# Optimization experiments

Measured on AMD Instinct MI355X. Metric: run time of the kernel, lower is better.

Reference implementation:

```python
import jax, jax.numpy as jnp
import numpy as np

B, N, ND, H = 8, 1024, 64, 128
NUM_OPS, NUM_PARAMS, SKETCH = 64, 256, 128


def setup_inputs() -> dict:
    key = jax.random.key(0)
    ks = iter(jax.random.split(key, 64))

    def rn(shape, s=0.05):
        return jax.random.normal(next(ks), shape, dtype=jnp.float32) * s

    inp = {
        'node_features': jax.random.normal(next(ks), (B, N, ND), dtype=jnp.float32),
        'adjacency': (jax.random.uniform(next(ks), (B, N, N)) < 0.05).astype(jnp.float32),
        'mask': jnp.ones((B, N), jnp.float32),
    }
    for name, din in (('g1', ND), ('g2', H), ('g3', H)):
        inp[name + '_W'] = rn((din, H))
        inp[name + '_b'] = jnp.zeros((H,), jnp.float32)
        inp[name + '_aW'] = rn((2 * H,))
        inp[name + '_ab'] = jnp.zeros((), jnp.float32)
    for l in (0, 1):
        inp[f'l{l}_Wih'] = rn((4 * H, H))
        inp[f'l{l}_Whh'] = rn((4 * H, H))
        inp[f'l{l}_bih'] = jnp.zeros((4 * H,), jnp.float32)
        inp[f'l{l}_bhh'] = jnp.zeros((4 * H,), jnp.float32)
    for name, dout in (('op', NUM_OPS), ('pa', NUM_PARAMS), ('sk', SKETCH), ('no', ND)):
        inp[name + '_W1'] = rn((H, H))
        inp[name + '_b1'] = jnp.zeros((H,), jnp.float32)
        inp[name + '_W2'] = rn((H, dout))
        inp[name + '_b2'] = jnp.zeros((dout,), jnp.float32)
    return inp


def _gnn(x, adj, W, b, aW, ab):
    # h = Linear(x); att[b,i,j] = sigmoid(aW . [h_j ; h_i] + ab)  (cat order from the torch code)
    h = x @ W + b                      # [B,N,H]
    D = W.shape[1]
    sj = h @ aW[:D]                    # contribution of the dim-1-expanded term (h_j)
    si = h @ aW[D:]                    # contribution of the dim-2-expanded term (h_i)
    att = jax.nn.sigmoid(si[:, :, None] + sj[:, None, :] + ab) * adj  # [B,N,N]
    return jnp.einsum('bij,bjd->bid', att, h)


def _lstm(x, Wih, Whh, bih, bhh):
    # single torch-style LSTM layer, gate order i,f,g,o; zero initial state
    Bx, Hh = x.shape[0], Whh.shape[1]

    def step(carry, xt):
        h, c = carry
        g = xt @ Wih.T + h @ Whh.T + (bih + bhh)       # [B,4H]
        i, f, gg, o = jnp.split(g, 4, axis=-1)
        c = jax.nn.sigmoid(f) * c + jax.nn.sigmoid(i) * jnp.tanh(gg)
        h = jax.nn.sigmoid(o) * jnp.tanh(c)
        return (h, c), h

    z = jnp.zeros((Bx, Hh), x.dtype)
    _, ys = jax.lax.scan(step, (z, z), jnp.swapaxes(x, 0, 1))
    return jnp.swapaxes(ys, 0, 1)


def _mlp(x, W1, b1, W2, b2):
    return jax.nn.relu(x @ W1 + b1) @ W2 + b2


def reference(node_features, adjacency, mask,
              g1_W, g1_b, g1_aW, g1_ab,
              g2_W, g2_b, g2_aW, g2_ab,
              g3_W, g3_b, g3_aW, g3_ab,
              l0_Wih, l0_Whh, l0_bih, l0_bhh,
              l1_Wih, l1_Whh, l1_bih, l1_bhh,
              op_W1, op_b1, op_W2, op_b2,
              pa_W1, pa_b1, pa_W2, pa_b2,
              sk_W1, sk_b1, sk_W2, sk_b2,
              no_W1, no_b1, no_W2, no_b2):
    h = jax.nn.relu(_gnn(node_features, adjacency, g1_W, g1_b, g1_aW, g1_ab))
    h = jax.nn.relu(_gnn(h, adjacency, g2_W, g2_b, g2_aW, g2_ab))
    h = _gnn(h, adjacency, g3_W, g3_b, g3_aW, g3_ab)
    lo = _lstm(h, l0_Wih, l0_Whh, l0_bih, l0_bhh)
    lo = _lstm(lo, l1_Wih, l1_Whh, l1_bih, l1_bhh)
    op_pred = _mlp(lo, op_W1, op_b1, op_W2, op_b2)
    param_pred = _mlp(lo, pa_W1, pa_b1, pa_W2, pa_b2)
    sketch_pred = _mlp(lo, sk_W1, sk_b1, sk_W2, sk_b2)
    node_pred = _mlp(h, no_W1, no_b1, no_W2, no_b2)
    return (op_pred, param_pred, sketch_pred, node_pred)
```

## Files before the change

### kernel.cpp

```cpp
#include <hip/hip_runtime.h>
#include <hip/hip_fp16.h>

typedef __attribute__((ext_vector_type(8))) short short8;
typedef __attribute__((ext_vector_type(4))) float f32x4;
typedef __attribute__((ext_vector_type(2))) unsigned int u32x2;

__device__ __forceinline__ unsigned short bf16_of(float f) {
    unsigned u = __builtin_bit_cast(unsigned, f);
    u += 0x7fffu + ((u >> 16) & 1u);
    return (unsigned short)(u >> 16);
}
__device__ __forceinline__ unsigned bf16pk(float a, float b) {
    return (unsigned)bf16_of(a) | ((unsigned)bf16_of(b) << 16);
}
__device__ __forceinline__ unsigned fp16pk(float a, float b) {
    return __builtin_bit_cast(unsigned, __builtin_amdgcn_cvt_pkrtz(a, b));
}
__device__ __forceinline__ f32x4 h4f(u32x2 v) {
    __half2 a = __builtin_bit_cast(__half2, v[0]);
    __half2 b = __builtin_bit_cast(__half2, v[1]);
    float2 fa = __half22float2(a), fb = __half22float2(b);
    f32x4 r; r[0] = fa.x; r[1] = fa.y; r[2] = fb.x; r[3] = fb.y;
    return r;
}
__device__ __forceinline__ float fexp2(float x) { return __builtin_amdgcn_exp2f(x); }
__device__ __forceinline__ float frcp(float x) { return __builtin_amdgcn_rcpf(x); }
__device__ __forceinline__ float sigm(float x) { return frcp(1.f + fexp2(-1.44269504f * x)); }
__device__ __forceinline__ f32x4 mfma16(short8 a, short8 b, f32x4 c) {
    return __builtin_amdgcn_mfma_f32_16x16x32_bf16(a, b, c, 0, 0, 0);
}
__device__ __forceinline__ float dpp_shr8(float x) {
    return __builtin_bit_cast(float, __builtin_amdgcn_update_dpp(
        0, __builtin_bit_cast(int, x), 0x118, 0xF, 0xF, true));
}
__device__ __forceinline__ float dpp_shl8(float x) {
    return __builtin_bit_cast(float, __builtin_amdgcn_update_dpp(
        0, __builtin_bit_cast(int, x), 0x108, 0xF, 0xF, true));
}

__global__ __launch_bounds__(256) void gemm_f32(
    const float* __restrict__ A, const float* __restrict__ B,
    const float* __restrict__ bias, float* __restrict__ C,
    int M, int N, int K, int BT, int RELU, int PACK)
{
    __shared__ float As[64][33];
    __shared__ float Bs[32][68];
    const int tid = threadIdx.x;
    const int tx = tid & 15, ty = tid >> 4;
    const int m0 = blockIdx.y * 64, n0 = blockIdx.x * 64;
    float acc[4][4];
#pragma unroll
    for (int i = 0; i < 4; ++i)
#pragma unroll
        for (int j = 0; j < 4; ++j) acc[i][j] = 0.f;

    for (int k0 = 0; k0 < K; k0 += 32) {
        __syncthreads();
        {
            const int r = tid >> 2, kk = (tid & 3) * 8;
            const float* src = A + (size_t)(m0 + r) * K + k0 + kk;
            f32x4 v0 = *(const f32x4*)src;
            f32x4 v1 = *(const f32x4*)(src + 4);
#pragma unroll
            for (int e = 0; e < 4; ++e) { As[r][kk + e] = v0[e]; As[r][kk + 4 + e] = v1[e]; }
        }
        if (!BT) {
            const int kk = tid >> 3, nn = (tid & 7) * 8;
            const float* src = B + (size_t)(k0 + kk) * N + n0 + nn;
            f32x4 v0 = *(const f32x4*)src;
            f32x4 v1 = *(const f32x4*)(src + 4);
#pragma unroll
            for (int e = 0; e < 4; ++e) { Bs[kk][nn + e] = v0[e]; Bs[kk][nn + 4 + e] = v1[e]; }
        } else {
            const int n = tid >> 2, kk = (tid & 3) * 8;
            const float* src = B + (size_t)(n0 + n) * K + k0 + kk;
            f32x4 v0 = *(const f32x4*)src;
            f32x4 v1 = *(const f32x4*)(src + 4);
#pragma unroll
            for (int e = 0; e < 4; ++e) { Bs[kk + e][n] = v0[e]; Bs[kk + 4 + e][n] = v1[e]; }
        }
        __syncthreads();
#pragma unroll 8
        for (int k = 0; k < 32; ++k) {
            float a0 = As[ty * 4 + 0][k], a1 = As[ty * 4 + 1][k];
            float a2 = As[ty * 4 + 2][k], a3 = As[ty * 4 + 3][k];
            f32x4 bv = *(const f32x4*)&Bs[k][tx * 4];
#pragma unroll
            for (int j = 0; j < 4; ++j) {
                acc[0][j] += a0 * bv[j]; acc[1][j] += a1 * bv[j];
                acc[2][j] += a2 * bv[j]; acc[3][j] += a3 * bv[j];
            }
        }
    }
    f32x4 bv = {};
    if (bias != nullptr) bv = *(const f32x4*)&bias[n0 + tx * 4];
#pragma unroll
    for (int i = 0; i < 4; ++i) {
        f32x4 res = {};
#pragma unroll
        for (int j = 0; j < 4; ++j) {
            float v = acc[i][j] + bv[j];
            if (RELU) v = fmaxf(v, 0.f);
            res[j] = v;
        }
        const int m = m0 + ty * 4 + i;
        if (!PACK) {
            *(f32x4*)&C[(size_t)m * N + n0 + tx * 4] = res;
        } else {
            const int b = m >> 10, t = m & 1023;
            const int n = n0 + tx * 4;
            const int pr = n >> 7, h = n & 127;
            if (pr == 3) {
#pragma unroll
                for (int j = 0; j < 4; ++j) res[j] *= 0.5f;
            }
            __half* Ch = (__half*)C;
            u32x2 ov = {fp16pk(res[0], res[1]), fp16pk(res[2], res[3])};
            *(u32x2*)&Ch[(((size_t)t * 4 + pr) * 8 + b) * 128 + h] = ov;
        }
    }
}

__global__ __launch_bounds__(256) void gemm_gnn(
    const float* __restrict__ A, const float* __restrict__ B,
    const float* __restrict__ bias, const float* __restrict__ aW,
    unsigned short* __restrict__ hT, float* __restrict__ siP,
    float* __restrict__ sjP, int K)
{
    __shared__ float As[64][33];
    __shared__ float Bs[32][68];
    __shared__ unsigned short T[64][70];
    const int tid = threadIdx.x;
    const int tx = tid & 15, ty = tid >> 4;
    const int m0 = blockIdx.y * 64, n0 = blockIdx.x * 64;
    float acc[4][4];
#pragma unroll
    for (int i = 0; i < 4; ++i)
#pragma unroll
        for (int j = 0; j < 4; ++j) acc[i][j] = 0.f;

    for (int k0 = 0; k0 < K; k0 += 32) {
        __syncthreads();
        {
            const int r = tid >> 2, kk = (tid & 3) * 8;
            const float* src = A + (size_t)(m0 + r) * K + k0 + kk;
            f32x4 v0 = *(const f32x4*)src;
            f32x4 v1 = *(const f32x4*)(src + 4);
#pragma unroll
            for (int e = 0; e < 4; ++e) { As[r][kk + e] = v0[e]; As[r][kk + 4 + e] = v1[e]; }
        }
        {
            const int kk = tid >> 3, nn = (tid & 7) * 8;
            const float* src = B + (size_t)(k0 + kk) * 128 + n0 + nn;
            f32x4 v0 = *(const f32x4*)src;
            f32x4 v1 = *(const f32x4*)(src + 4);
#pragma unroll
            for (int e = 0; e < 4; ++e) { Bs[kk][nn + e] = v0[e]; Bs[kk][nn + 4 + e] = v1[e]; }
        }
        __syncthreads();
#pragma unroll 8
        for (int k = 0; k < 32; ++k) {
            float a0 = As[ty * 4 + 0][k], a1 = As[ty * 4 + 1][k];
            float a2 = As[ty * 4 + 2][k], a3 = As[ty * 4 + 3][k];
            f32x4 bv = *(const f32x4*)&Bs[k][tx * 4];
#pragma unroll
            for (int j = 0; j < 4; ++j) {
                acc[0][j] += a0 * bv[j]; acc[1][j] += a1 * bv[j];
                acc[2][j] += a2 * bv[j]; acc[3][j] += a3 * bv[j];
            }
        }
    }
    f32x4 bv = *(const f32x4*)&bias[n0 + tx * 4];
#pragma unroll
    for (int i = 0; i < 4; ++i)
#pragma unroll
        for (int j = 0; j < 4; ++j) acc[i][j] += bv[j];

    f32x4 wj = *(const f32x4*)&aW[n0 + tx * 4];
    f32x4 wi = *(const f32x4*)&aW[128 + n0 + tx * 4];
#pragma unroll
    for (int i = 0; i < 4; ++i) {
        float pj = acc[i][0] * wj[0] + acc[i][1] * wj[1] + acc[i][2] * wj[2] + acc[i][3] * wj[3];
        float pi = acc[i][0] * wi[0] + acc[i][1] * wi[1] + acc[i][2] * wi[2] + acc[i][3] * wi[3];
#pragma unroll
        for (int o = 8; o > 0; o >>= 1) {
            pj += __shfl_xor(pj, o);
            pi += __shfl_xor(pi, o);
        }
        if (tx == 0) {
            const int m = m0 + ty * 4 + i;
            sjP[blockIdx.x * 8192 + m] = pj;
            siP[blockIdx.x * 8192 + m] = pi;
        }
    }

#pragma unroll
    for (int i = 0; i < 4; ++i) {
        unsigned* tp = (unsigned*)&T[ty * 4 + i][tx * 4];
        tp[0] = bf16pk(acc[i][0], acc[i][1]);
        tp[1] = bf16pk(acc[i][2], acc[i][3]);
    }
    __syncthreads();
    const int b = m0 >> 10, node0 = m0 & 1023;
    const int r = tid >> 4, c4 = (tid & 15) * 4;
#pragma unroll
    for (int rr = 0; rr < 4; ++rr) {
        const int d = rr * 16 + r;
        u32x2 o;
        o[0] = (unsigned)T[c4 + 0][d] | ((unsigned)T[c4 + 1][d] << 16);
        o[1] = (unsigned)T[c4 + 2][d] | ((unsigned)T[c4 + 3][d] << 16);
        *(u32x2*)(hT + ((size_t)b * 128 + n0 + d) * 1024 + node0 + c4) = o;
    }
}

__global__ __launch_bounds__(256) void gnn_agg(
    const float* __restrict__ adj, const unsigned short* __restrict__ hT,
    const float* __restrict__ siP, const float* __restrict__ sjP,
    const float* __restrict__ abp, float* __restrict__ out, int RELU)
{
    __shared__ __align__(16) unsigned short Alds[32 * 40];
    __shared__ __align__(16) unsigned short Blds[128 * 40];
    __shared__ float sjL[1024];
    const int b = blockIdx.y, it = blockIdx.x;
    const int i0 = it * 32;
    const int tid = threadIdx.x, lane = tid & 63, w = tid >> 6;
    const int quad = lane >> 4, col = lane & 15;
    const int rh = w & 1, nh = w >> 1;
    const float ab = abp[0];
    const float* adjb = adj + (size_t)b * 1024 * 1024;
    const unsigned short* hTb = hT + (size_t)b * 128 * 1024;

    for (int j = tid; j < 1024; j += 256)
        sjL[j] = sjP[b * 1024 + j] + sjP[8192 + b * 1024 + j];

    const int ar_ = tid >> 3, ash = (tid & 7) * 4;
    const int br_ = tid >> 1, bsh = (tid & 1) * 16;
    const float sii = siP[b * 1024 + i0 + ar_] + siP[8192 + b * 1024 + i0 + ar_] + ab;

    const float* aptr = adjb + (size_t)(i0 + ar_) * 1024 + ash;
    const unsigned short* bptr = hTb + (size_t)br_ * 1024 + bsh;

    f32x4 paA = *(const f32x4*)(aptr);
    short8 pbA0 = *(const short8*)(bptr);
    short8 pbA1 = *(const short8*)(bptr + 8);
    f32x4 paB = *(const f32x4*)(aptr + 32);
    short8 pbB0 = *(const short8*)(bptr + 32);
    short8 pbB1 = *(const short8*)(bptr + 40);

    f32x4 acc[4] = {};

    for (int j0 = 0; j0 < 1024; j0 += 64) {
        __syncthreads();
        {
            float s0 = sigm(sii + sjL[j0 + ash + 0]) * paA[0];
            float s1 = sigm(sii + sjL[j0 + ash + 1]) * paA[1];
            float s2 = sigm(sii + sjL[j0 + ash + 2]) * paA[2];
            float s3 = sigm(sii + sjL[j0 + ash + 3]) * paA[3];
            u32x2 o = {bf16pk(s0, s1), bf16pk(s2, s3)};
            *(u32x2*)&Alds[ar_ * 40 + ash] = o;
            *(short8*)&Blds[br_ * 40 + bsh] = pbA0;
            *(short8*)&Blds[br_ * 40 + bsh + 8] = pbA1;
        }
        if (j0 + 64 < 1024) {
            paA = *(const f32x4*)(aptr + j0 + 64);
            pbA0 = *(const short8*)(bptr + j0 + 64);
            pbA1 = *(const short8*)(bptr + j0 + 72);
        }
        __syncthreads();
        {
            short8 af = *(const short8*)&Alds[(rh * 16 + col) * 40 + quad * 8];
#pragma unroll
            for (int nt = 0; nt < 4; ++nt) {
                short8 bf = *(const short8*)&Blds[((nh * 4 + nt) * 16 + col) * 40 + quad * 8];
                acc[nt] = mfma16(af, bf, acc[nt]);
            }
        }
        __syncthreads();
        {
            float s0 = sigm(sii + sjL[j0 + 32 + ash + 0]) * paB[0];
            float s1 = sigm(sii + sjL[j0 + 32 + ash + 1]) * paB[1];
            float s2 = sigm(sii + sjL[j0 + 32 + ash + 2]) * paB[2];
            float s3 = sigm(sii + sjL[j0 + 32 + ash + 3]) * paB[3];
            u32x2 o = {bf16pk(s0, s1), bf16pk(s2, s3)};
            *(u32x2*)&Alds[ar_ * 40 + ash] = o;
            *(short8*)&Blds[br_ * 40 + bsh] = pbB0;
            *(short8*)&Blds[br_ * 40 + bsh + 8] = pbB1;
        }
        if (j0 + 96 < 1024) {
            paB = *(const f32x4*)(aptr + j0 + 96);
            pbB0 = *(const short8*)(bptr + j0 + 96);
            pbB1 = *(const short8*)(bptr + j0 + 104);
        }
        __syncthreads();
        {
            short8 af = *(const short8*)&Alds[(rh * 16 + col) * 40 + quad * 8];
#pragma unroll
            for (int nt = 0; nt < 4; ++nt) {
                short8 bf = *(const short8*)&Blds[((nh * 4 + nt) * 16 + col) * 40 + quad * 8];
                acc[nt] = mfma16(af, bf, acc[nt]);
            }
        }
    }
    const int ibase = i0 + rh * 16 + quad * 4;
#pragma unroll
    for (int nt = 0; nt < 4; ++nt) {
        const int d = (nh * 4 + nt) * 16 + col;
#pragma unroll
        for (int r = 0; r < 4; ++r) {
            float v = acc[nt][r];
            if (RELU) v = fmaxf(v, 0.f);
            out[((size_t)b * 1024 + ibase + r) * 128 + d] = v;
        }
    }
}

struct PrepArgs {
    const float* src[8];
    unsigned short* dst[8];
    int N[8];
};
__global__ __launch_bounds__(256) void prep_k(
    PrepArgs pa, const float* bih0, const float* bhh0,
    float* bsum, int* flags)
{
    const int m = blockIdx.x;
    const int tid = threadIdx.x;
    if (m < 8) {
        const float* src = pa.src[m];
        unsigned short* dst = pa.dst[m];
        const int N = pa.N[m];
        const int n0 = tid >> 4, kc = (tid & 15) * 8;
        for (int n = n0; n < N; n += 16) {
            unsigned o[4];
#pragma unroll
            for (int e = 0; e < 8; e += 2)
                o[e >> 1] = bf16pk(src[(size_t)(kc + e) * N + n],
                                   src[(size_t)(kc + e + 1) * N + n]);
            *(u32x2*)&dst[n * 128 + kc] = *(u32x2*)&o[0];
            *(u32x2*)&dst[n * 128 + kc + 4] = *(u32x2*)&o[2];
        }
    } else {
        bsum[tid] = bih0[tid] + bhh0[tid];
        bsum[tid + 256] = bih0[tid + 256] + bhh0[tid + 256];
        if (tid < 3) flags[tid] = 0;
    }
}


struct HeadArgs {
    const unsigned short* W1T[4];
    const float* b1[4];
    const unsigned short* W2T[4];
    const float* b2[4];
    float* outp[4];
};

__device__ __forceinline__ void lstm_epilogue(
    const f32x4 accs[4], f32x4 xv0, f32x4 xv1, float* cst, float* hv,
    bool lo, float selLo)
{
    float t0[4], t1[4];
#pragma unroll
    for (int i = 0; i < 4; ++i) {
        float P0 = (lo ? accs[0][i] : dpp_shr8(accs[1][i])) + xv0[i];
        float P1 = (lo ? accs[2][i] : dpp_shr8(accs[3][i])) + xv1[i];
        P1 = fmaxf(P1, -30.f);
        t0[i] = frcp(1.f + fexp2(-1.44269504f * P0));
        float u = fexp2(-2.88539008f * P1);
        t1[i] = (1.f - selLo * u) * frcp(1.f + u);
    }
    float c2[4], og[4];
#pragma unroll
    for (int i = 0; i < 4; ++i) {
        float ig = t0[i];
        float fg = dpp_shl8(t0[i]);
        float gg = t1[i];
        og[i] = dpp_shl8(t1[i]);
        c2[i] = fg * cst[i] + ig * gg;
        cst[i] = c2[i];
    }
    float pc0 = lo ? c2[0] : dpp_shr8(c2[1]);
    float pc1 = lo ? c2[2] : dpp_shr8(c2[3]);
    pc0 = fmaxf(pc0, -30.f);
    pc1 = fmaxf(pc1, -30.f);
    float u0 = fexp2(-2.88539008f * pc0);
    float tc0 = (1.f - u0) * frcp(1.f + u0);
    float u1 = fexp2(-2.88539008f * pc1);
    float tc1 = (1.f - u1) * frcp(1.f + u1);
    float th[4] = {tc0, dpp_shl8(tc0), tc1, dpp_shl8(tc1)};
#pragma unroll
    for (int i = 0; i < 4; ++i) hv[i] = og[i] * th[i];
}

template <int SINK>
__device__ __forceinline__ void lstm_step(
    unsigned short* Hc, unsigned short* Hn, const short8 afr[4][4],
    f32x4 xv0, f32x4 xv1, float* cst, unsigned short* __restrict__ sink,
    int t, int col, int quad, int h4, int b)
{
    short8 bfr[4];
#pragma unroll
    for (int c = 0; c < 4; ++c)
        bfr[c] = *(const short8*)&Hc[col * 136 + c * 32 + quad * 8];
    f32x4 accs[4] = {};
#pragma unroll
    for (int c = 0; c < 4; ++c)
#pragma unroll
        for (int g = 0; g < 4; ++g)
            accs[g] = mfma16(afr[g][c], bfr[c], accs[g]);

    const bool lo = (col < 8);
    const float selLo = lo ? 1.f : 0.f;
    float hv[4];
    lstm_epilogue(accs, xv0, xv1, cst, hv, lo, selLo);
    if (lo) {
        u32x2 hb = {bf16pk(hv[0], hv[1]), bf16pk(hv[2], hv[3])};
        *(u32x2*)&Hn[b * 136 + h4] = hb;
        if (SINK == 0)
            *(u32x2*)(sink + (size_t)t * 1024 + b * 128 + h4) = hb;
        else
            *(u32x2*)(sink + ((size_t)t * 8 + b) * 128 + h4) = hb;
    }
    __builtin_amdgcn_s_waitcnt(0xC07F);
    __builtin_amdgcn_s_barrier();
}

template <int A32, int LROWS>
__device__ void head_strip(
    const void* __restrict__ Asrc, int row0,
    const unsigned short* __restrict__ W1T, const float* __restrict__ b1,
    const unsigned short* __restrict__ W2T, const float* __restrict__ b2,
    float* __restrict__ outp, int dout, unsigned short* A2, int tid)
{
    const int lane = tid & 63, w = tid >> 6;
    const int quad = lane >> 4, col = lane & 15;
    const int mrow = w * 16 + col;
    f32x4 acc[8] = {};
#pragma unroll
    for (int kc = 0; kc < 4; ++kc) {
        short8 af;
        if (A32) {
            const float* s = (const float*)Asrc + (size_t)(row0 + mrow) * 128 + kc * 32 + quad * 8;
            f32x4 v0 = *(const f32x4*)s, v1 = *(const f32x4*)(s + 4);
            short8 v;
#pragma unroll
            for (int j = 0; j < 4; ++j) {
                v[j] = (short)bf16_of(v0[j]);
                v[4 + j] = (short)bf16_of(v1[j]);
            }
            af = v;
        } else {
            af = *(const short8*)((const unsigned short*)Asrc +
                                  (size_t)(row0 + mrow) * 128 + kc * 32 + quad * 8);
        }
#pragma unroll
        for (int nt = 0; nt < 8; ++nt) {
            short8 bf = *(const short8*)&W1T[(nt * 16 + col) * 128 + kc * 32 + quad * 8];
            acc[nt] = mfma16(af, bf, acc[nt]);
        }
    }
    float b1v[8];
#pragma unroll
    for (int nt = 0; nt < 8; ++nt) b1v[nt] = b1[nt * 16 + col];
    __syncthreads();
#pragma unroll
    for (int nt = 0; nt < 8; ++nt)
#pragma unroll
        for (int i = 0; i < 4; ++i) {
            const int mm = w * 16 + quad * 4 + i;
            A2[mm * 136 + nt * 16 + col] = bf16_of(fmaxf(acc[nt][i] + b1v[nt], 0.f));
        }
    __syncthreads();
    const int ntiles = dout >> 4;
    for (int np = 0; np < ntiles; np += 8) {
        const int nts = (ntiles - np < 8) ? ntiles - np : 8;
        f32x4 acc2[8] = {};
#pragma unroll
        for (int kc = 0; kc < 4; ++kc) {
            short8 a2f = *(const short8*)&A2[mrow * 136 + kc * 32 + quad * 8];
            for (int nt = 0; nt < nts; ++nt) {
                short8 bf = *(const short8*)&W2T[((np + nt) * 16 + col) * 128 + kc * 32 + quad * 8];
                acc2[nt] = mfma16(a2f, bf, acc2[nt]);
            }
        }
        for (int nt = 0; nt < nts; ++nt) {
            const int n = (np + nt) * 16 + col;
            const float bb = b2[n];
#pragma unroll
            for (int i = 0; i < 4; ++i) {
                const int r = row0 + w * 16 + quad * 4 + i;
                size_t off;
                if (LROWS) off = ((size_t)(r & 7) * 1024 + (r >> 3)) * dout + n;
                else       off = (size_t)r * dout + n;
                outp[off] = acc2[nt][i] + bb;
            }
        }
    }
}

__global__ __launch_bounds__(512, 2) void lstm_pipe(
    const __half* __restrict__ xw0, const float* __restrict__ Whh0,
    const float* __restrict__ Wih1, const float* __restrict__ Whh1,
    const float* __restrict__ bih1, const float* __restrict__ bhh1,
    unsigned short* __restrict__ hbuf, __half* __restrict__ xw1,
    int* __restrict__ flags, unsigned short* __restrict__ out1b,
    const float* __restrict__ bufH3, HeadArgs ha)
{
    __shared__ __align__(16) unsigned short H[2][16 * 136];
    __shared__ __align__(16) unsigned short A2[128 * 136];
    const int tid = threadIdx.x;
    const int lane = tid & 63;
    const int w = tid >> 6;
    const int quad = lane >> 4;
    const int col = lane & 15;
    const int b = col & 7;
    const int prA = col >> 3;
    const int h4 = w * 16 + quad * 4;

    if (blockIdx.x >= 3) {
        const int wid = blockIdx.x - 3;
        for (int s = wid; s < 64; s += 8)
            head_strip<1, 0>(bufH3, s * 128, ha.W1T[3], ha.b1[3],
                             ha.W2T[3], ha.b2[3], ha.outp[3], 64, A2, tid);
        for (int s = wid; s < 64; s += 8) {
            if (tid == 0) {
                while (__hip_atomic_load(&flags[2], __ATOMIC_ACQUIRE,
                                         __HIP_MEMORY_SCOPE_AGENT) < s + 1)
                    __builtin_amdgcn_s_sleep(16);
            }
            __syncthreads();
            head_strip<0, 1>(out1b, s * 128, ha.W1T[0], ha.b1[0],
                             ha.W2T[0], ha.b2[0], ha.outp[0], 64, A2, tid);
            head_strip<0, 1>(out1b, s * 128, ha.W1T[1], ha.b1[1],
                             ha.W2T[1], ha.b2[1], ha.outp[1], 256, A2, tid);
            head_strip<0, 1>(out1b, s * 128, ha.W1T[2], ha.b1[2],
                             ha.W2T[2], ha.b2[2], ha.outp[2], 128, A2, tid);
        }
        return;
    }

    if (blockIdx.x == 1) {
        short8 afrI[4][4];
        f32x4 biasv[4];
#pragma unroll
        for (int g = 0; g < 4; ++g) {
            const float gsc = (g == 3) ? 0.5f : 1.f;
            const int row = g * 128 + w * 16 + col;
#pragma unroll
            for (int c = 0; c < 4; ++c) {
                const float* src = Wih1 + row * 128 + c * 32 + quad * 8;
                short8 v;
#pragma unroll
                for (int j = 0; j < 8; ++j) v[j] = (short)bf16_of(src[j] * gsc);
                afrI[g][c] = v;
            }
            const int rb = g * 128 + w * 16 + quad * 4;
            f32x4 b1 = *(const f32x4*)&bih1[rb];
            f32x4 b2 = *(const f32x4*)&bhh1[rb];
#pragma unroll
            for (int e = 0; e < 4; ++e) biasv[g][e] = (b1[e] + b2[e]) * gsc;
        }
        for (int k = 0; k < 64; ++k) {
            if (tid == 0) {
                while (__hip_atomic_load(&flags[0], __ATOMIC_ACQUIRE,
                                         __HIP_MEMORY_SCOPE_AGENT) < k + 1)
                    __builtin_amdgcn_s_sleep(2);
                if (k >= 4) {
                    while (__hip_atomic_load(&flags[2], __ATOMIC_RELAXED,
                                             __HIP_MEMORY_SCOPE_AGENT) < k - 3)
                        __builtin_amdgcn_s_sleep(2);
                }
            }
            __builtin_amdgcn_s_waitcnt(0xC07F);
            __builtin_amdgcn_s_barrier();
            const unsigned short* hb = hbuf + (size_t)k * 16 * 1024;
            __half* dst = xw1 + (size_t)(k & 3) * 65536;
#pragma unroll 2
            for (int nt = 0; nt < 8; ++nt) {
                const int tl = nt * 2 + (col >> 3);
                const unsigned short* src = hb + tl * 1024 + b * 128 + quad * 8;
                short8 bfr[4];
#pragma unroll
                for (int c = 0; c < 4; ++c) bfr[c] = *(const short8*)&src[c * 32];
                f32x4 acc[4] = {};
#pragma unroll
                for (int c = 0; c < 4; ++c)
#pragma unroll
                    for (int g = 0; g < 4; ++g)
                        acc[g] = mfma16(afrI[g][c], bfr[c], acc[g]);
#pragma unroll
                for (int g = 0; g < 4; ++g) {
                    u32x2 res = {fp16pk(acc[g][0] + biasv[g][0], acc[g][1] + biasv[g][1]),
                                 fp16pk(acc[g][2] + biasv[g][2], acc[g][3] + biasv[g][3])};
                    *(u32x2*)&dst[((tl * 4 + g) * 8 + b) * 128 + w * 16 + quad * 4] = res;
                }
            }
            __builtin_amdgcn_s_waitcnt(0x0F70);
            __builtin_amdgcn_s_barrier();
            if (tid == 0)
                __hip_atomic_store(&flags[1], k + 1, __ATOMIC_RELEASE,
                                   __HIP_MEMORY_SCOPE_AGENT);
        }
        return;
    }

    for (int i = tid; i < 2 * 16 * 136; i += 512) (&H[0][0])[i] = 0;
    float cst[4] = {0.f, 0.f, 0.f, 0.f};
    const int lane_off = (prA * 8 + b) * 128 + h4;

    if (blockIdx.x == 0) {
        short8 afr[4][4];
#pragma unroll
        for (int g = 0; g < 4; ++g) {
            const float gsc = (g == 3) ? 0.5f : 1.f;
            const int row = g * 128 + w * 16 + col;
#pragma unroll
            for (int c = 0; c < 4; ++c) {
                const float* src = Whh0 + row * 128 + c * 32 + quad * 8;
                short8 v;
#pragma unroll
                for (int j = 0; j < 8; ++j) v[j] = (short)bf16_of(src[j] * gsc);
                afr[g][c] = v;
            }
        }
        const __half* xp = xw0 + lane_off;
        u32x2 p0a = *(const u32x2*)(xp);
        u32x2 p1a = *(const u32x2*)(xp + 2048);
        u32x2 p0b = *(const u32x2*)(xp + 4096);
        u32x2 p1b = *(const u32x2*)(xp + 6144);
        xp += 8192;
        __syncthreads();

        for (int t = 0; t < 1024; t += 2) {
            const __half* xr = (t == 1022) ? xp - 8192 : xp;
            {
                f32x4 xv0 = h4f(p0a), xv1 = h4f(p1a);
                p0a = *(const u32x2*)(xr);
                p1a = *(const u32x2*)(xr + 2048);
                lstm_step<0>(&H[0][0], &H[1][0], afr, xv0, xv1, cst, hbuf, t, col, quad, h4, b);
            }
            {
                f32x4 xv0 = h4f(p0b), xv1 = h4f(p1b);
                p0b = *(const u32x2*)(xr + 4096);
                p1b = *(const u32x2*)(xr + 6144);
                lstm_step<0>(&H[1][0], &H[0][0], afr, xv0, xv1, cst, hbuf, t + 1, col, quad, h4, b);
            }
            xp += 8192;
            if ((t & 14) == 14) {
                __syncthreads();
                if (tid == 0)
                    __hip_atomic_store(&flags[0], (t >> 4) + 1, __ATOMIC_RELEASE,
                                       __HIP_MEMORY_SCOPE_AGENT);
            }
        }
    } else {
        short8 afr[4][4];
#pragma unroll
        for (int g = 0; g < 4; ++g) {
            const float gsc = (g == 3) ? 0.5f : 1.f;
            const int row = g * 128 + w * 16 + col;
#pragma unroll
            for (int c = 0; c < 4; ++c) {
                const float* src = Whh1 + row * 128 + c * 32 + quad * 8;
                short8 v;
#pragma unroll
                for (int j = 0; j < 8; ++j) v[j] = (short)bf16_of(src[j] * gsc);
                afr[g][c] = v;
            }
        }
        __syncthreads();
        auto xaddr = [&](int t) -> const __half* {
            return xw1 + (((t >> 4) & 3) * 65536 + (t & 15) * 4096) + lane_off;
        };
        while (__hip_atomic_load(&flags[1], __ATOMIC_ACQUIRE,
                                 __HIP_MEMORY_SCOPE_AGENT) < 2)
            __builtin_amdgcn_s_sleep(2);
        u32x2 p0a = *(const u32x2*)xaddr(0);
        u32x2 p1a = *(const u32x2*)(xaddr(0) + 2048);
        u32x2 p0b = *(const u32x2*)xaddr(1);
        u32x2 p1b = *(const u32x2*)(xaddr(1) + 2048);

        for (int c = 0; c < 64; ++c) {
            if (c > 0) {
                const int target = (c + 2 < 64) ? c + 2 : 64;
                if (tid == 0) {
                    while (__hip_atomic_load(&flags[1], __ATOMIC_ACQUIRE,
                                             __HIP_MEMORY_SCOPE_AGENT) < target)
                        __builtin_amdgcn_s_sleep(2);
                }
                __builtin_amdgcn_s_waitcnt(0xC07F);
                __builtin_amdgcn_s_barrier();
            }
            for (int s = 0; s < 16; s += 2) {
                const int t = c * 16 + s;
                const int t2 = (t + 2 < 1024) ? t + 2 : 1023;
                const int t3 = (t + 3 < 1024) ? t + 3 : 1023;
                {
                    f32x4 xv0 = h4f(p0a), xv1 = h4f(p1a);
                    p0a = *(const u32x2*)xaddr(t2);
                    p1a = *(const u32x2*)(xaddr(t2) + 2048);
                    lstm_step<1>(&H[0][0], &H[1][0], afr, xv0, xv1, cst, out1b, t, col, quad, h4, b);
                }
                {
                    f32x4 xv0 = h4f(p0b), xv1 = h4f(p1b);
                    p0b = *(const u32x2*)xaddr(t3);
                    p1b = *(const u32x2*)(xaddr(t3) + 2048);
                    lstm_step<1>(&H[1][0], &H[0][0], afr, xv0, xv1, cst, out1b, t + 1, col, quad, h4, b);
                }
            }
            __syncthreads();
            if (tid == 0)
                __hip_atomic_store(&flags[2], c + 1, __ATOMIC_RELEASE,
                                   __HIP_MEMORY_SCOPE_AGENT);
        }
    }
}

extern "C" void kernel_launch(void* const* d_in, const int* in_sizes, int n_in,
                              void* d_out, int out_size, void* d_ws, size_t ws_size,
                              hipStream_t stream)
{
    (void)in_sizes; (void)n_in; (void)out_size; (void)ws_size;
    const float* nf    = (const float*)d_in[0];
    const float* adj   = (const float*)d_in[1];
    const float* g1W   = (const float*)d_in[3];
    const float* g1b   = (const float*)d_in[4];
    const float* g1aW  = (const float*)d_in[5];
    const float* g1ab  = (const float*)d_in[6];
    const float* g2W   = (const float*)d_in[7];
    const float* g2b   = (const float*)d_in[8];
    const float* g2aW  = (const float*)d_in[9];
    const float* g2ab  = (const float*)d_in[10];
    const float* g3W   = (const float*)d_in[11];
    const float* g3b   = (const float*)d_in[12];
    const float* g3aW  = (const float*)d_in[13];
    const float* g3ab  = (const float*)d_in[14];
    const float* l0Wih = (const float*)d_in[15];
    const float* l0Whh = (const float*)d_in[16];
    const float* l0bih = (const float*)d_in[17];
    const float* l0bhh = (const float*)d_in[18];
    const float* l1Wih = (const float*)d_in[19];
    const float* l1Whh = (const float*)d_in[20];
    const float* l1bih = (const float*)d_in[21];
    const float* l1bhh = (const float*)d_in[22];
    const float* opW1 = (const float*)d_in[23];
    const float* opb1 = (const float*)d_in[24];
    const float* opW2 = (const float*)d_in[25];
    const float* opb2 = (const float*)d_in[26];
    const float* paW1 = (const float*)d_in[27];
    const float* pab1 = (const float*)d_in[28];
    const float* paW2 = (const float*)d_in[29];
    const float* pab2 = (const float*)d_in[30];
    const float* skW1 = (const float*)d_in[31];
    const float* skb1 = (const float*)d_in[32];
    const float* skW2 = (const float*)d_in[33];
    const float* skb2 = (const float*)d_in[34];
    const float* noW1 = (const float*)d_in[35];
    const float* nob1 = (const float*)d_in[36];
    const float* noW2 = (const float*)d_in[37];
    const float* nob2 = (const float*)d_in[38];

    float* out = (float*)d_out;
    float* ws = (float*)d_ws;
    float* siP   = ws;
    float* sjP   = ws + 16384;
    float* bufX  = ws + 1048576;
    float* bufH3 = ws + 2097152;
    unsigned short* bufT = (unsigned short*)(ws + 3145728);
    float* bsum = ws + 3686400;
    float* xw0f = ws + 3687424;
    float* xw1f = ws + 7881728;
    int*  flags = (int*)(ws + 8143872);
    unsigned short* WT = (unsigned short*)(ws + 8143876);
    unsigned short* out1b = (unsigned short*)(ws + 8209412);
    unsigned short* hbuf = (unsigned short*)bufX;
    __half* xw0 = (__half*)xw0f;
    __half* xw1 = (__half*)xw1f;

    unsigned short* opW1T = WT;
    unsigned short* paW1T = WT + 16384;
    unsigned short* skW1T = WT + 32768;
    unsigned short* noW1T = WT + 49152;
    unsigned short* opW2T = WT + 65536;
    unsigned short* paW2T = WT + 73728;
    unsigned short* skW2T = WT + 106496;
    unsigned short* noW2T = WT + 122880;

    gemm_gnn<<<dim3(2, 128), 256, 0, stream>>>(nf, g1W, g1b, g1aW, bufT, siP, sjP, 64);
    gnn_agg<<<dim3(32, 8), 256, 0, stream>>>(adj, bufT, siP, sjP, g1ab, bufX, 1);
    gemm_gnn<<<dim3(2, 128), 256, 0, stream>>>(bufX, g2W, g2b, g2aW, bufT, siP, sjP, 128);
    gnn_agg<<<dim3(32, 8), 256, 0, stream>>>(adj, bufT, siP, sjP, g2ab, bufX, 1);
    gemm_gnn<<<dim3(2, 128), 256, 0, stream>>>(bufX, g3W, g3b, g3aW, bufT, siP, sjP, 128);
    gnn_agg<<<dim3(32, 8), 256, 0, stream>>>(adj, bufT, siP, sjP, g3ab, bufH3, 0);

    PrepArgs pargs;
    pargs.src[0] = opW1; pargs.dst[0] = opW1T; pargs.N[0] = 128;
    pargs.src[1] = paW1; pargs.dst[1] = paW1T; pargs.N[1] = 128;
    pargs.src[2] = skW1; pargs.dst[2] = skW1T; pargs.N[2] = 128;
    pargs.src[3] = noW1; pargs.dst[3] = noW1T; pargs.N[3] = 128;
    pargs.src[4] = opW2; pargs.dst[4] = opW2T; pargs.N[4] = 64;
    pargs.src[5] = paW2; pargs.dst[5] = paW2T; pargs.N[5] = 256;
    pargs.src[6] = skW2; pargs.dst[6] = skW2T; pargs.N[6] = 128;
    pargs.src[7] = noW2; pargs.dst[7] = noW2T; pargs.N[7] = 64;
    prep_k<<<9, 256, 0, stream>>>(pargs, l0bih, l0bhh, bsum, flags);

    {
        dim3 g(512 / 64, 8192 / 64);
        gemm_f32<<<g, dim3(256), 0, stream>>>(bufH3, l0Wih, bsum, (float*)xw0,
                                              8192, 512, 128, 1, 0, 1);
    }

    HeadArgs ha;
    ha.W1T[0] = opW1T; ha.b1[0] = opb1; ha.W2T[0] = opW2T; ha.b2[0] = opb2;
    ha.outp[0] = out + 0;
    ha.W1T[1] = paW1T; ha.b1[1] = pab1; ha.W2T[1] = paW2T; ha.b2[1] = pab2;
    ha.outp[1] = out + 524288;
    ha.W1T[2] = skW1T; ha.b1[2] = skb1; ha.W2T[2] = skW2T; ha.b2[2] = skb2;
    ha.outp[2] = out + 2621440;
    ha.W1T[3] = noW1T; ha.b1[3] = nob1; ha.W2T[3] = noW2T; ha.b2[3] = nob2;
    ha.outp[3] = out + 3670016;
    lstm_pipe<<<11, 512, 0, stream>>>(xw0, l0Whh, l1Wih, l1Whh, l1bih, l1bhh,
                                      hbuf, xw1, flags, out1b, bufH3, ha);
}
```

Before: 1.333 ms.

## Fuse GNN layers, weight prep and LSTM input projection into one cooperative kernel

Replaces the six GNN kernel launches, the prep kernel and the fp32 input-projection GEMM with a single cooperative persistent kernel of 256 blocks that uses grid-wide syncs between phases. The weight transposes and the Wih bf16 conversion now run in the same phase as the third GNN GEMM. The LSTM layer-0 input projection is redone with bf16 MFMA instead of the fp32 SIMT GEMM. This is meant to remove launch gaps and speed up the projection, at the cost of grid-sync overhead, a shared-memory union that may lower occupancy, and bf16 rounding of h3 and Wih.

```diff
diff --git a/kernel.cpp b/kernel.cpp
--- a/kernel.cpp
+++ b/kernel.cpp
@@ -1,5 +1,8 @@
 #include <hip/hip_runtime.h>
 #include <hip/hip_fp16.h>
+#include <hip/hip_cooperative_groups.h>
+
+namespace cg = cooperative_groups;
 
 typedef __attribute__((ext_vector_type(8))) short short8;
 typedef __attribute__((ext_vector_type(4))) float f32x4;
@@ -38,16 +41,28 @@
         0, __builtin_bit_cast(int, x), 0x108, 0xF, 0xF, true));
 }
 
-__global__ __launch_bounds__(256) void gemm_f32(
+struct SmemG { float As[64][33]; float Bs[32][68]; unsigned short T[64][70]; };
+struct SmemA { unsigned short Alds[32 * 40]; unsigned short Blds[128 * 40]; float sjL[1024]; };
+struct SmemP { unsigned short hA[64 * 136]; };
+union SmemU { SmemG g; SmemA a; SmemP p; };
+
+struct PrepArgs {
+    const float* src[8];
+    unsigned short* dst[8];
+    int N[8];
+};
+
+__device__ void gemm_gnn_dev(
     const float* __restrict__ A, const float* __restrict__ B,
-    const float* __restrict__ bias, float* __restrict__ C,
-    int M, int N, int K, int BT, int RELU, int PACK)
-{
-    __shared__ float As[64][33];
-    __shared__ float Bs[32][68];
-    const int tid = threadIdx.x;
+    const float* __restrict__ bias, const float* __restrict__ aW,
+    unsigned short* __restrict__ hT, float* __restrict__ siP,
+    float* __restrict__ sjP, int K, int bx, int by, SmemG* sg, int tid)
+{
+    float (*As)[33] = sg->As;
+    float (*Bs)[68] = sg->Bs;
+    unsigned short (*T)[70] = sg->T;
     const int tx = tid & 15, ty = tid >> 4;
-    const int m0 = blockIdx.y * 64, n0 = blockIdx.x * 64;
+    const int m0 = by * 64, n0 = bx * 64;
     float acc[4][4];
 #pragma unroll
     for (int i = 0; i < 4; ++i)
@@ -64,20 +79,13 @@
 #pragma unroll
             for (int e = 0; e < 4; ++e) { As[r][kk + e] = v0[e]; As[r][kk + 4 + e] = v1[e]; }
         }
-        if (!BT) {
+        {
             const int kk = tid >> 3, nn = (tid & 7) * 8;
-            const float* src = B + (size_t)(k0 + kk) * N + n0 + nn;
+            const float* src = B + (size_t)(k0 + kk) * 128 + n0 + nn;
             f32x4 v0 = *(const f32x4*)src;
             f32x4 v1 = *(const f32x4*)(src + 4);
 #pragma unroll
             for (int e = 0; e < 4; ++e) { Bs[kk][nn + e] = v0[e]; Bs[kk][nn + 4 + e] = v1[e]; }
-        } else {
-            const int n = tid >> 2, kk = (tid & 3) * 8;
-            const float* src = B + (size_t)(n0 + n) * K + k0 + kk;
-            f32x4 v0 = *(const f32x4*)src;
-            f32x4 v1 = *(const f32x4*)(src + 4);
-#pragma unroll
-            for (int e = 0; e < 4; ++e) { Bs[kk + e][n] = v0[e]; Bs[kk + 4 + e][n] = v1[e]; }
         }
         __syncthreads();
 #pragma unroll 8
@@ -92,84 +100,6 @@
             }
         }
     }
-    f32x4 bv = {};
-    if (bias != nullptr) bv = *(const f32x4*)&bias[n0 + tx * 4];
-#pragma unroll
-    for (int i = 0; i < 4; ++i) {
-        f32x4 res = {};
-#pragma unroll
-        for (int j = 0; j < 4; ++j) {
-            float v = acc[i][j] + bv[j];
-            if (RELU) v = fmaxf(v, 0.f);
-            res[j] = v;
-        }
-        const int m = m0 + ty * 4 + i;
-        if (!PACK) {
-            *(f32x4*)&C[(size_t)m * N + n0 + tx * 4] = res;
-        } else {
-            const int b = m >> 10, t = m & 1023;
-            const int n = n0 + tx * 4;
-            const int pr = n >> 7, h = n & 127;
-            if (pr == 3) {
-#pragma unroll
-                for (int j = 0; j < 4; ++j) res[j] *= 0.5f;
-            }
-            __half* Ch = (__half*)C;
-            u32x2 ov = {fp16pk(res[0], res[1]), fp16pk(res[2], res[3])};
-            *(u32x2*)&Ch[(((size_t)t * 4 + pr) * 8 + b) * 128 + h] = ov;
-        }
-    }
-}
-
-__global__ __launch_bounds__(256) void gemm_gnn(
-    const float* __restrict__ A, const float* __restrict__ B,
-    const float* __restrict__ bias, const float* __restrict__ aW,
-    unsigned short* __restrict__ hT, float* __restrict__ siP,
-    float* __restrict__ sjP, int K)
-{
-    __shared__ float As[64][33];
-    __shared__ float Bs[32][68];
-    __shared__ unsigned short T[64][70];
-    const int tid = threadIdx.x;
-    const int tx = tid & 15, ty = tid >> 4;
-    const int m0 = blockIdx.y * 64, n0 = blockIdx.x * 64;
-    float acc[4][4];
-#pragma unroll
-    for (int i = 0; i < 4; ++i)
-#pragma unroll
-        for (int j = 0; j < 4; ++j) acc[i][j] = 0.f;
-
-    for (int k0 = 0; k0 < K; k0 += 32) {
-        __syncthreads();
-        {
-            const int r = tid >> 2, kk = (tid & 3) * 8;
-            const float* src = A + (size_t)(m0 + r) * K + k0 + kk;
-            f32x4 v0 = *(const f32x4*)src;
-            f32x4 v1 = *(const f32x4*)(src + 4);
-#pragma unroll
-            for (int e = 0; e < 4; ++e) { As[r][kk + e] = v0[e]; As[r][kk + 4 + e] = v1[e]; }
-        }
-        {
-            const int kk = tid >> 3, nn = (tid & 7) * 8;
-            const float* src = B + (size_t)(k0 + kk) * 128 + n0 + nn;
-            f32x4 v0 = *(const f32x4*)src;
-            f32x4 v1 = *(const f32x4*)(src + 4);
-#pragma unroll
-            for (int e = 0; e < 4; ++e) { Bs[kk][nn + e] = v0[e]; Bs[kk][nn + 4 + e] = v1[e]; }
-        }
-        __syncthreads();
-#pragma unroll 8
-        for (int k = 0; k < 32; ++k) {
-            float a0 = As[ty * 4 + 0][k], a1 = As[ty * 4 + 1][k];
-            float a2 = As[ty * 4 + 2][k], a3 = As[ty * 4 + 3][k];
-            f32x4 bv = *(const f32x4*)&Bs[k][tx * 4];
-#pragma unroll
-            for (int j = 0; j < 4; ++j) {
-                acc[0][j] += a0 * bv[j]; acc[1][j] += a1 * bv[j];
-                acc[2][j] += a2 * bv[j]; acc[3][j] += a3 * bv[j];
-            }
-        }
-    }
     f32x4 bv = *(const f32x4*)&bias[n0 + tx * 4];
 #pragma unroll
     for (int i = 0; i < 4; ++i)
@@ -189,8 +119,8 @@
         }
         if (tx == 0) {
             const int m = m0 + ty * 4 + i;
-            sjP[blockIdx.x * 8192 + m] = pj;
-            siP[blockIdx.x * 8192 + m] = pi;
+            sjP[bx * 8192 + m] = pj;
+            siP[bx * 8192 + m] = pi;
         }
     }
 
@@ -213,17 +143,17 @@
     }
 }
 
-__global__ __launch_bounds__(256) void gnn_agg(
+__device__ void gnn_agg_dev(
     const float* __restrict__ adj, const unsigned short* __restrict__ hT,
     const float* __restrict__ siP, const float* __restrict__ sjP,
-    const float* __restrict__ abp, float* __restrict__ out, int RELU)
-{
-    __shared__ __align__(16) unsigned short Alds[32 * 40];
-    __shared__ __align__(16) unsigned short Blds[128 * 40];
-    __shared__ float sjL[1024];
-    const int b = blockIdx.y, it = blockIdx.x;
+    const float* __restrict__ abp, float* __restrict__ out, int RELU,
+    int it, int b, SmemA* sa, int tid)
+{
+    unsigned short* Alds = sa->Alds;
+    unsigned short* Blds = sa->Blds;
+    float* sjL = sa->sjL;
     const int i0 = it * 32;
-    const int tid = threadIdx.x, lane = tid & 63, w = tid >> 6;
+    const int lane = tid & 63, w = tid >> 6;
     const int quad = lane >> 4, col = lane & 15;
     const int rh = w & 1, nh = w >> 1;
     const float ab = abp[0];
@@ -314,36 +244,143 @@
     }
 }
 
-struct PrepArgs {
-    const float* src[8];
-    unsigned short* dst[8];
-    int N[8];
+__device__ void prep_transpose_dev(const float* __restrict__ src,
+                                   unsigned short* __restrict__ dst,
+                                   int N, int tid)
+{
+    const int n0 = tid >> 4, kc = (tid & 15) * 8;
+    for (int n = n0; n < N; n += 16) {
+        unsigned o[4];
+#pragma unroll
+        for (int e = 0; e < 8; e += 2)
+            o[e >> 1] = bf16pk(src[(size_t)(kc + e) * N + n],
+                               src[(size_t)(kc + e + 1) * N + n]);
+        *(u32x2*)&dst[n * 128 + kc] = *(u32x2*)&o[0];
+        *(u32x2*)&dst[n * 128 + kc + 4] = *(u32x2*)&o[2];
+    }
+}
+
+__device__ void wih_convert_dev(const float* __restrict__ src,
+                                unsigned short* __restrict__ dst,
+                                int base, int tid)
+{
+    for (int i = tid * 8; i < 16384; i += 2048) {
+        const float* s = src + base + i;
+        f32x4 v0 = *(const f32x4*)s, v1 = *(const f32x4*)(s + 4);
+        short8 o;
+#pragma unroll
+        for (int j = 0; j < 4; ++j) {
+            o[j] = (short)bf16_of(v0[j]);
+            o[4 + j] = (short)bf16_of(v1[j]);
+        }
+        *(short8*)(dst + base + i) = o;
+    }
+}
+
+__device__ void pack_dev(const float* __restrict__ h3,
+                         const unsigned short* __restrict__ WihB,
+                         const float* __restrict__ bih, const float* __restrict__ bhh,
+                         __half* __restrict__ xw0, int bid, SmemP* sp, int tid)
+{
+    const int row0 = bid * 64;
+    const int lane = tid & 63, w = tid >> 6;
+    const int quad = lane >> 4, col = lane & 15;
+    {
+        const int r = tid >> 2, c0 = (tid & 3) * 32;
+        const float* src = h3 + (size_t)(row0 + r) * 128 + c0;
+        unsigned short* dst = sp->hA + r * 136 + c0;
+#pragma unroll
+        for (int e = 0; e < 32; e += 8) {
+            f32x4 v0 = *(const f32x4*)(src + e);
+            f32x4 v1 = *(const f32x4*)(src + e + 4);
+            short8 o;
+#pragma unroll
+            for (int j = 0; j < 4; ++j) {
+                o[j] = (short)bf16_of(v0[j]);
+                o[4 + j] = (short)bf16_of(v1[j]);
+            }
+            *(short8*)(dst + e) = o;
+        }
+    }
+    __syncthreads();
+    float bs[8];
+#pragma unroll
+    for (int nt = 0; nt < 8; ++nt) {
+        const int n = w * 128 + nt * 16 + col;
+        bs[nt] = bih[n] + bhh[n];
+    }
+    const float gsc = (w == 3) ? 0.5f : 1.f;
+#pragma unroll
+    for (int rt = 0; rt < 4; ++rt) {
+        short8 af[4];
+#pragma unroll
+        for (int c = 0; c < 4; ++c)
+            af[c] = *(const short8*)&sp->hA[(rt * 16 + col) * 136 + c * 32 + quad * 8];
+        f32x4 acc[8] = {};
+#pragma unroll
+        for (int c = 0; c < 4; ++c)
+#pragma unroll
+            for (int nt = 0; nt < 8; ++nt) {
+                short8 bf = *(const short8*)&WihB[(size_t)(w * 128 + nt * 16 + col) * 128 + c * 32 + quad * 8];
+                acc[nt] = mfma16(af[c], bf, acc[nt]);
+            }
+#pragma unroll
+        for (int nt = 0; nt < 8; ++nt)
+#pragma unroll
+            for (int i = 0; i < 4; ++i) {
+                const int m = row0 + rt * 16 + quad * 4 + i;
+                const int bq = m >> 10, t = m & 1023;
+                const float v = (acc[nt][i] + bs[nt]) * gsc;
+                xw0[(((size_t)t * 4 + w) * 8 + bq) * 128 + nt * 16 + col] = (__half)v;
+            }
+    }
+}
+
+struct MegaArgs {
+    const float* nf; const float* adj;
+    const float* gW[3]; const float* gb[3];
+    const float* gaW[3]; const float* gab[3];
+    const float* l0Wih; const float* l0bih; const float* l0bhh;
+    unsigned short* hT; float* siP; float* sjP;
+    float* bufX; float* bufH3;
+    __half* xw0; unsigned short* WihB; int* flags;
+    PrepArgs prep;
 };
-__global__ __launch_bounds__(256) void prep_k(
-    PrepArgs pa, const float* bih0, const float* bhh0,
-    float* bsum, int* flags)
-{
-    const int m = blockIdx.x;
+
+__global__ __launch_bounds__(256) void gnn_mega(MegaArgs a)
+{
+    __shared__ __align__(16) SmemU sm;
+    const int bid = blockIdx.x;
     const int tid = threadIdx.x;
-    if (m < 8) {
-        const float* src = pa.src[m];
-        unsigned short* dst = pa.dst[m];
-        const int N = pa.N[m];
-        const int n0 = tid >> 4, kc = (tid & 15) * 8;
-        for (int n = n0; n < N; n += 16) {
-            unsigned o[4];
-#pragma unroll
-            for (int e = 0; e < 8; e += 2)
-                o[e >> 1] = bf16pk(src[(size_t)(kc + e) * N + n],
-                                   src[(size_t)(kc + e + 1) * N + n]);
-            *(u32x2*)&dst[n * 128 + kc] = *(u32x2*)&o[0];
-            *(u32x2*)&dst[n * 128 + kc + 4] = *(u32x2*)&o[2];
-        }
-    } else {
-        bsum[tid] = bih0[tid] + bhh0[tid];
-        bsum[tid + 256] = bih0[tid + 256] + bhh0[tid + 256];
-        if (tid < 3) flags[tid] = 0;
-    }
+    cg::grid_group grid = cg::this_grid();
+
+    gemm_gnn_dev(a.nf, a.gW[0], a.gb[0], a.gaW[0], a.hT, a.siP, a.sjP, 64,
+                 bid & 1, bid >> 1, &sm.g, tid);
+    grid.sync();
+    gnn_agg_dev(a.adj, a.hT, a.siP, a.sjP, a.gab[0], a.bufX, 1,
+                bid & 31, bid >> 5, &sm.a, tid);
+    grid.sync();
+    gemm_gnn_dev(a.bufX, a.gW[1], a.gb[1], a.gaW[1], a.hT, a.siP, a.sjP, 128,
+                 bid & 1, bid >> 1, &sm.g, tid);
+    grid.sync();
+    gnn_agg_dev(a.adj, a.hT, a.siP, a.sjP, a.gab[1], a.bufX, 1,
+                bid & 31, bid >> 5, &sm.a, tid);
+    grid.sync();
+    gemm_gnn_dev(a.bufX, a.gW[2], a.gb[2], a.gaW[2], a.hT, a.siP, a.sjP, 128,
+                 bid & 1, bid >> 1, &sm.g, tid);
+    if (bid < 8) {
+        prep_transpose_dev(a.prep.src[bid], a.prep.dst[bid], a.prep.N[bid], tid);
+    } else if (bid < 12) {
+        wih_convert_dev(a.l0Wih, a.WihB, (bid - 8) * 16384, tid);
+    } else if (bid == 12 && tid < 3) {
+        a.flags[tid] = 0;
+    }
+    grid.sync();
+    gnn_agg_dev(a.adj, a.hT, a.siP, a.sjP, a.gab[2], a.bufH3, 0,
+                bid & 31, bid >> 5, &sm.a, tid);
+    grid.sync();
+    if (bid < 128)
+        pack_dev(a.bufH3, a.WihB, a.l0bih, a.l0bhh, a.xw0, bid, &sm.p, tid);
 }
 
 
@@ -764,10 +801,10 @@
     float* ws = (float*)d_ws;
     float* siP   = ws;
     float* sjP   = ws + 16384;
+    unsigned short* WihB = (unsigned short*)(ws + 40960);
     float* bufX  = ws + 1048576;
     float* bufH3 = ws + 2097152;
     unsigned short* bufT = (unsigned short*)(ws + 3145728);
-    float* bsum = ws + 3686400;
     float* xw0f = ws + 3687424;
     float* xw1f = ws + 7881728;
     int*  flags = (int*)(ws + 8143872);
@@ -786,29 +823,25 @@
     unsigned short* skW2T = WT + 106496;
     unsigned short* noW2T = WT + 122880;
 
-    gemm_gnn<<<dim3(2, 128), 256, 0, stream>>>(nf, g1W, g1b, g1aW, bufT, siP, sjP, 64);
-    gnn_agg<<<dim3(32, 8), 256, 0, stream>>>(adj, bufT, siP, sjP, g1ab, bufX, 1);
-    gemm_gnn<<<dim3(2, 128), 256, 0, stream>>>(bufX, g2W, g2b, g2aW, bufT, siP, sjP, 128);
-    gnn_agg<<<dim3(32, 8), 256, 0, stream>>>(adj, bufT, siP, sjP, g2ab, bufX, 1);
-    gemm_gnn<<<dim3(2, 128), 256, 0, stream>>>(bufX, g3W, g3b, g3aW, bufT, siP, sjP, 128);
-    gnn_agg<<<dim3(32, 8), 256, 0, stream>>>(adj, bufT, siP, sjP, g3ab, bufH3, 0);
-
-    PrepArgs pargs;
-    pargs.src[0] = opW1; pargs.dst[0] = opW1T; pargs.N[0] = 128;
-    pargs.src[1] = paW1; pargs.dst[1] = paW1T; pargs.N[1] = 128;
-    pargs.src[2] = skW1; pargs.dst[2] = skW1T; pargs.N[2] = 128;
-    pargs.src[3] = noW1; pargs.dst[3] = noW1T; pargs.N[3] = 128;
-    pargs.src[4] = opW2; pargs.dst[4] = opW2T; pargs.N[4] = 64;
-    pargs.src[5] = paW2; pargs.dst[5] = paW2T; pargs.N[5] = 256;
-    pargs.src[6] = skW2; pargs.dst[6] = skW2T; pargs.N[6] = 128;
-    pargs.src[7] = noW2; pargs.dst[7] = noW2T; pargs.N[7] = 64;
-    prep_k<<<9, 256, 0, stream>>>(pargs, l0bih, l0bhh, bsum, flags);
-
-    {
-        dim3 g(512 / 64, 8192 / 64);
-        gemm_f32<<<g, dim3(256), 0, stream>>>(bufH3, l0Wih, bsum, (float*)xw0,
-                                              8192, 512, 128, 1, 0, 1);
-    }
+    MegaArgs ma;
+    ma.nf = nf; ma.adj = adj;
+    ma.gW[0] = g1W; ma.gb[0] = g1b; ma.gaW[0] = g1aW; ma.gab[0] = g1ab;
+    ma.gW[1] = g2W; ma.gb[1] = g2b; ma.gaW[1] = g2aW; ma.gab[1] = g2ab;
+    ma.gW[2] = g3W; ma.gb[2] = g3b; ma.gaW[2] = g3aW; ma.gab[2] = g3ab;
+    ma.l0Wih = l0Wih; ma.l0bih = l0bih; ma.l0bhh = l0bhh;
+    ma.hT = bufT; ma.siP = siP; ma.sjP = sjP;
+    ma.bufX = bufX; ma.bufH3 = bufH3;
+    ma.xw0 = xw0; ma.WihB = WihB; ma.flags = flags;
+    ma.prep.src[0] = opW1; ma.prep.dst[0] = opW1T; ma.prep.N[0] = 128;
+    ma.prep.src[1] = paW1; ma.prep.dst[1] = paW1T; ma.prep.N[1] = 128;
+    ma.prep.src[2] = skW1; ma.prep.dst[2] = skW1T; ma.prep.N[2] = 128;
+    ma.prep.src[3] = noW1; ma.prep.dst[3] = noW1T; ma.prep.N[3] = 128;
+    ma.prep.src[4] = opW2; ma.prep.dst[4] = opW2T; ma.prep.N[4] = 64;
+    ma.prep.src[5] = paW2; ma.prep.dst[5] = paW2T; ma.prep.N[5] = 256;
+    ma.prep.src[6] = skW2; ma.prep.dst[6] = skW2T; ma.prep.N[6] = 128;
+    ma.prep.src[7] = noW2; ma.prep.dst[7] = noW2T; ma.prep.N[7] = 64;
+    void* params[] = { &ma };
+    hipLaunchCooperativeKernel(gnn_mega, dim3(256), dim3(256), params, 0, stream);
 
     HeadArgs ha;
     ha.W1T[0] = opW1T; ha.b1[0] = opb1; ha.W2T[0] = opW2T; ha.b2[0] = opb2;
```

Measured after the change: 1.546 ms. 15.9% more time.
